# Optimization experiments

Measured on AMD Instinct MI355X. Metric: run time of the kernel, lower is better.

The kernel has to match this reference:

```python
import jax, jax.numpy as jnp
import numpy as np

EPS = 1e-5
NEG_INF = -9e15  # matches torch's -9000000000000000.0 mask fill


def layer_norm(x, g, b):
    mu = jnp.mean(x, axis=-1, keepdims=True)
    var = jnp.mean((x - mu) ** 2, axis=-1, keepdims=True)
    return (x - mu) / jnp.sqrt(var + EPS) * g + b


def setup_inputs() -> dict:
    key = jax.random.key(0)
    n, C, Cout, K = 8192, 128, 128, 2
    ks = jax.random.split(key, 5)
    x = jax.random.normal(ks[0], (n, C), dtype=jnp.float32)
    adj = jax.random.randint(ks[1], (n, n), 0, 2).astype(jnp.float32)  # 0/1 adjacency
    s = 1.0 / np.sqrt(C)
    # W0[i]: applied as h = x @ W0[i]  (== torch Linear(C,C,bias=False))
    W0 = jax.random.uniform(ks[2], (K, C, C), dtype=jnp.float32, minval=-s, maxval=s)
    W1 = jax.random.uniform(ks[3], (K, C, Cout), dtype=jnp.float32, minval=-s, maxval=s)
    sa = 1.0 / np.sqrt(2 * C)
    a = jax.random.uniform(ks[4], (K, 2 * C), dtype=jnp.float32, minval=-sa, maxval=sa)
    ln1_g = jnp.ones((C,), jnp.float32); ln1_b = jnp.zeros((C,), jnp.float32)
    ln2_g = jnp.ones((C,), jnp.float32); ln2_b = jnp.zeros((C,), jnp.float32)
    return {"x": x, "adj": adj, "W0": W0, "W1": W1, "a": a,
            "ln1_g": ln1_g, "ln1_b": ln1_b, "ln2_g": ln2_g, "ln2_b": ln2_b}


def reference(x, adj, W0, W1, a, ln1_g, ln1_b, ln2_g, ln2_b):
    n, C = x.shape
    K = W0.shape[0]
    Cout = W1.shape[-1]
    # adj + eye (repeated) only feeds `> 0`; equivalent fixed mask:
    mask = (adj > 0) | jnp.eye(n, dtype=bool)
    x_norm = layer_norm(x, ln1_g, ln1_b)
    h_next = jnp.zeros((n, Cout), dtype=x.dtype)
    atten_agg = jnp.zeros((n, n), dtype=x.dtype)
    for i in range(K):
        h = x_norm @ W0[i]                                   # (n, C)
        a_l, a_r = a[i, :C], a[i, C:]
        # h_cross[i,j] = [h[i], h[j]]; linear decomposes exactly:
        e = jax.nn.leaky_relu(h @ a_l[:, None] + (h @ a_r)[None, :])  # (n, n)
        e = jnp.where(mask, e, NEG_INF)
        atten = jax.nn.softmax(e, axis=1)                    # row-stochastic
        attn_h = atten @ h                                   # (n, C)
        attn_h = attn_h + x                                  # residual=True
        attn_h = layer_norm(attn_h, ln2_g, ln2_b)
        h_next = h_next + jax.nn.elu(attn_h @ W1[i]) / K
        atten_agg = atten_agg + atten / K
    return h_next, atten_agg
```

## Files before the change

kernel.cpp:

```cpp
#include <hip/hip_runtime.h>
#include <stdint.h>

#define N 8192
#define C 128

typedef float f32x4 __attribute__((ext_vector_type(4)));
typedef short bf16x8 __attribute__((ext_vector_type(8)));

__device__ __forceinline__ float wred(float v){
#pragma unroll
  for(int o=32;o;o>>=1) v += __shfl_xor(v,o);
  return v;
}
__device__ __forceinline__ unsigned short f2bf(float x){
  union{float f; unsigned u;} c; c.f = x;
  unsigned u = c.u;
  u += 0x7fffu + ((u>>16)&1u);
  return (unsigned short)(u>>16);
}
__device__ __forceinline__ float lrelu(float z){ return z>0.f ? z : 0.01f*z; }

__global__ void k_front(const float* __restrict__ x, const float* __restrict__ g1,
                        const float* __restrict__ b1, const float* __restrict__ W0,
                        const float* __restrict__ a, unsigned short* __restrict__ hB,
                        float* __restrict__ hl, float* __restrict__ hr){
  __shared__ __align__(16) float xn[32*132];
  __shared__ __align__(16) float ws[C*C];
  __shared__ __align__(16) float hs[32*C];
  int t = threadIdx.x, l = t & 63, w = t >> 6;
  int r0 = blockIdx.x*32;
#pragma unroll
  for(int p=0;p<8;p++){
    int row = p*4 + w;
    const float2 xv = *(const float2*)(x + (size_t)(r0+row)*C + l*2);
    float mu = wred(xv.x + xv.y) * (1.f/C);
    float dx = xv.x - mu, dy = xv.y - mu;
    float var = wred(dx*dx + dy*dy) * (1.f/C);
    float rs = rsqrtf(var + 1e-5f);
    const float2 gv = *(const float2*)(g1 + l*2);
    const float2 bv = *(const float2*)(b1 + l*2);
    xn[row*132 + l*2]     = dx*rs*gv.x + bv.x;
    xn[row*132 + l*2 + 1] = dy*rs*gv.y + bv.y;
  }
  int cq = t & 31, rq = t >> 5;
  for(int k=0;k<2;k++){
    __syncthreads();
    const float4* wsrc = (const float4*)(W0 + (size_t)k*C*C);
    float4* wdst = (float4*)ws;
#pragma unroll
    for(int r=0;r<16;r++) wdst[t + r*256] = wsrc[t + r*256];
    __syncthreads();
    float4 acc[4] = {};
    const float4* ws4 = (const float4*)ws;
#pragma unroll 4
    for(int kk=0; kk<C; ++kk){
      float4 wv = ws4[kk*32 + cq];
#pragma unroll
      for(int r=0;r<4;r++){
        float xv = xn[(rq*4+r)*132 + kk];
        acc[r].x += xv*wv.x; acc[r].y += xv*wv.y; acc[r].z += xv*wv.z; acc[r].w += xv*wv.w;
      }
    }
    const float4 al = *(const float4*)(a + k*2*C + cq*4);
    const float4 ar = *(const float4*)(a + k*2*C + C + cq*4);
#pragma unroll
    for(int r=0;r<4;r++){
      float sl = acc[r].x*al.x + acc[r].y*al.y + acc[r].z*al.z + acc[r].w*al.w;
      float sr = acc[r].x*ar.x + acc[r].y*ar.y + acc[r].z*ar.z + acc[r].w*ar.w;
#pragma unroll
      for(int o=16;o;o>>=1){ sl += __shfl_xor(sl,o); sr += __shfl_xor(sr,o); }
      if(cq==0){
        hl[k*N + r0 + rq*4 + r] = sl;
        hr[k*N + r0 + rq*4 + r] = sr;
      }
    }
#pragma unroll
    for(int r=0;r<4;r++) *(float4*)(hs + (rq*4+r)*C + cq*4) = acc[r];
    __syncthreads();
    unsigned short tv[16];
#pragma unroll
    for(int q=0;q<16;q++){
      int f = t*16 + q;
      int cb = f>>9, l2 = (f>>3)&63, tt = f&7;
      tv[q] = f2bf(hs[((l2>>4)*8 + tt)*C + cb*16 + (l2&15)]);
    }
    uint4* dst = (uint4*)(hB + (size_t)(k*256 + blockIdx.x)*4096 + t*16);
    dst[0] = *(uint4*)&tv[0];
    dst[1] = *(uint4*)&tv[8];
  }
}

__global__ void k_denom(const float* __restrict__ adj, const float* __restrict__ hl,
                        const float* __restrict__ hr, float* __restrict__ invd,
                        unsigned char* __restrict__ maskG){
  int t = threadIdx.x, l = t & 63, w = t >> 6;
  int i = blockIdx.x*8 + w;
  float hl0 = hl[i], hl1 = hl[N+i];
  const float4* arow = (const float4*)(adj + (size_t)i*N);
  float s0 = 0.f, s1 = 0.f;
  for(int it=0; it<16; ++it){
    int j0 = it*512 + l*8;
    float4 a0 = arow[j0/4], a1 = arow[j0/4 + 1];
    float4 h00 = *(const float4*)(hr + j0);
    float4 h01 = *(const float4*)(hr + j0 + 4);
    float4 h10 = *(const float4*)(hr + N + j0);
    float4 h11 = *(const float4*)(hr + N + j0 + 4);
    float av[8]  = {a0.x,a0.y,a0.z,a0.w, a1.x,a1.y,a1.z,a1.w};
    float h0v[8] = {h00.x,h00.y,h00.z,h00.w, h01.x,h01.y,h01.z,h01.w};
    float h1v[8] = {h10.x,h10.y,h10.z,h10.w, h11.x,h11.y,h11.z,h11.w};
    unsigned mb = 0;
#pragma unroll
    for(int tt=0; tt<8; ++tt){
      bool m = (av[tt] > 0.f) || (j0+tt == i);
      mb |= ((unsigned)m) << tt;
      float e0 = __expf(lrelu(hl0 + h0v[tt]));
      float e1 = __expf(lrelu(hl1 + h1v[tt]));
      s0 += m ? e0 : 0.f;
      s1 += m ? e1 : 0.f;
    }
    maskG[(size_t)i*1024 + it*64 + l] = (unsigned char)mb;
  }
  s0 = wred(s0); s1 = wred(s1);
  if(l==0){ invd[i] = 1.f/s0; invd[N+i] = 1.f/s1; }
}

__global__ __launch_bounds__(512, 4)
void k_main(const unsigned char* __restrict__ maskG, const float* __restrict__ hl,
            const float* __restrict__ hr, const float* __restrict__ invd,
            const unsigned short* __restrict__ hB,
            float* __restrict__ agg, float* __restrict__ pvp){
  __shared__ __align__(16) uint4 hBs[2][1024];
  __shared__ __align__(16) float hrs[2048];
  __shared__ __align__(16) unsigned char mlds[128*144];
  int t = threadIdx.x, l = t & 63, w = t >> 6;
  int r0 = blockIdx.x*128, ch = blockIdx.y;
  int g = l >> 4;
  int lr = w*16 + (l & 15);
  int i = r0 + lr;
  {
    int f0 = t*4, k0 = f0 >> 10, j0 = f0 & 1023;
    *(float4*)(hrs + f0) = *(const float4*)(hr + k0*N + ch*1024 + j0);
    const uint4* msrc = (const uint4*)(maskG + (size_t)(r0 + (t>>2))*1024 + ch*128 + (t&3)*32);
    uint4* mdst = (uint4*)(mlds + (t>>2)*144 + (t&3)*32);
    mdst[0] = msrc[0];
    mdst[1] = msrc[1];
  }
  float hl0 = hl[i], hl1 = hl[N+i];
  float id0 = invd[i], id1 = invd[N+i];
  float* grow = agg + (size_t)i*N;
  const uint4* hBu = (const uint4*)hB;
  f32x4 acc[2][8] = {};
  uint4 s0v, s1v;
  {
    size_t jn = (size_t)(ch*32)*512;
    s0v = hBu[jn + t];
    s1v = hBu[131072 + jn + t];
  }
  __syncthreads();
  int cur = 0;
  for(int js=0; js<32; ++js){
    int jblk = ch*32 + js;
    uint4* dstb = &hBs[cur][0];
    dstb[t      ] = s0v;
    dstb[t + 512] = s1v;
    if(js < 31){
      size_t jn = (size_t)(jblk+1)*512;
      s0v = hBu[jn + t];
      s1v = hBu[131072 + jn + t];
    }
    __syncthreads();
    int jb = jblk*32 + g*8;
    int jl = js*32 + g*8;
    float4 h00 = *(const float4*)(hrs + jl);
    float4 h01 = *(const float4*)(hrs + jl + 4);
    float4 h10 = *(const float4*)(hrs + 1024 + jl);
    float4 h11 = *(const float4*)(hrs + 1024 + jl + 4);
    unsigned mb = mlds[lr*144 + js*4 + g];
    float h0v[8] = {h00.x,h00.y,h00.z,h00.w, h01.x,h01.y,h01.z,h01.w};
    float h1v[8] = {h10.x,h10.y,h10.z,h10.w, h11.x,h11.y,h11.z,h11.w};
    float p0[8], p1[8];
#pragma unroll
    for(int tt=0; tt<8; ++tt){
      bool m = (mb >> tt) & 1;
      float e0 = __expf(lrelu(hl0 + h0v[tt]));
      float e1 = __expf(lrelu(hl1 + h1v[tt]));
      p0[tt] = m ? e0 : 0.f;
      p1[tt] = m ? e1 : 0.f;
    }
    float4 g0, g1;
    g0.x = (p0[0]*id0 + p1[0]*id1)*0.5f;
    g0.y = (p0[1]*id0 + p1[1]*id1)*0.5f;
    g0.z = (p0[2]*id0 + p1[2]*id1)*0.5f;
    g0.w = (p0[3]*id0 + p1[3]*id1)*0.5f;
    g1.x = (p0[4]*id0 + p1[4]*id1)*0.5f;
    g1.y = (p0[5]*id0 + p1[5]*id1)*0.5f;
    g1.z = (p0[6]*id0 + p1[6]*id1)*0.5f;
    g1.w = (p0[7]*id0 + p1[7]*id1)*0.5f;
    *(float4*)(grow + jb)     = g0;
    *(float4*)(grow + jb + 4) = g1;
    union { bf16x8 v; unsigned u[4]; } fu0, fu1;
#pragma unroll
    for(int q=0;q<4;q++){
      asm("v_cvt_pk_bf16_f32 %0, %1, %2" : "=v"(fu0.u[q]) : "v"(p0[2*q]), "v"(p0[2*q+1]));
      asm("v_cvt_pk_bf16_f32 %0, %1, %2" : "=v"(fu1.u[q]) : "v"(p1[2*q]), "v"(p1[2*q+1]));
    }
    const unsigned short* bptr = (const unsigned short*)&hBs[cur][0];
#pragma unroll
    for(int cb=0; cb<8; ++cb){
      bf16x8 b0 = *(const bf16x8*)(bptr + (cb*64 + l)*8);
      bf16x8 b1 = *(const bf16x8*)(bptr + 4096 + (cb*64 + l)*8);
      acc[0][cb] = __builtin_amdgcn_mfma_f32_16x16x32_bf16(fu0.v, b0, acc[0][cb], 0, 0, 0);
      acc[1][cb] = __builtin_amdgcn_mfma_f32_16x16x32_bf16(fu1.v, b1, acc[1][cb], 0, 0, 0);
    }
    __syncthreads();
    cur ^= 1;
  }
#pragma unroll
  for(int k=0;k<2;k++)
#pragma unroll
    for(int cb=0;cb<8;cb++)
#pragma unroll
      for(int r=0;r<4;r++){
        int ig = r0 + w*16 + ((l>>4)<<2) + r;
        int c = cb*16 + (l & 15);
        pvp[(size_t)((ch*2 + k)*N + ig)*C + c] = acc[k][cb][r];
      }
}

__global__ void k_reduce_ln(const float* __restrict__ pvp, const float* __restrict__ invd,
                            const float* __restrict__ x, const float* __restrict__ g2,
                            const float* __restrict__ b2, float* __restrict__ tmp){
  int l = threadIdx.x & 63, w = threadIdx.x >> 6;
  int wid = blockIdx.x*4 + w;
  int k = wid >> 13, i = wid & (N-1);
  float s0 = 0.f, s1 = 0.f;
#pragma unroll
  for(int ch=0; ch<8; ++ch){
    const float2 v = *(const float2*)(pvp + (size_t)((ch*2+k)*N + i)*C + l*2);
    s0 += v.x; s1 += v.y;
  }
  float idv = invd[k*N + i];
  const float2 xv = *(const float2*)(x + (size_t)i*C + l*2);
  float a0 = s0*idv + xv.x, a1 = s1*idv + xv.y;
  float mu = wred(a0 + a1) * (1.f/C);
  float d0 = a0 - mu, d1 = a1 - mu;
  float var = wred(d0*d0 + d1*d1) * (1.f/C);
  float rs = rsqrtf(var + 1e-5f);
  const float2 gv = *(const float2*)(g2 + l*2);
  const float2 bv = *(const float2*)(b2 + l*2);
  float2 o; o.x = d0*rs*gv.x + bv.x; o.y = d1*rs*gv.y + bv.y;
  *(float2*)(tmp + (size_t)k*N*C + (size_t)i*C + l*2) = o;
}

__global__ void k_out(const float* __restrict__ tmp, const float* __restrict__ W1,
                      float* __restrict__ out){
  __shared__ __align__(16) float ws[C*C];
  __shared__ __align__(16) float xs[32*132];
  int t = threadIdx.x, r0 = blockIdx.x*32;
  int cq = t & 31, rq = t >> 5;
  float oacc[4][4] = {};
  for(int k=0;k<2;k++){
    __syncthreads();
    const float4* wsrc = (const float4*)(W1 + (size_t)k*C*C);
    float4* wdst = (float4*)ws;
#pragma unroll
    for(int r=0;r<16;r++) wdst[t + r*256] = wsrc[t + r*256];
    const float4* xsrc = (const float4*)(tmp + (size_t)k*N*C + (size_t)r0*C);
#pragma unroll
    for(int r=0;r<4;r++){
      int f = t + r*256;
      int row = f >> 5, c4 = f & 31;
      *(float4*)(xs + row*132 + c4*4) = xsrc[f];
    }
    __syncthreads();
    float4 acc[4] = {};
    const float4* ws4 = (const float4*)ws;
#pragma unroll 4
    for(int kk=0; kk<C; ++kk){
      float4 wv = ws4[kk*32 + cq];
#pragma unroll
      for(int r=0;r<4;r++){
        float xv = xs[(rq*4+r)*132 + kk];
        acc[r].x += xv*wv.x; acc[r].y += xv*wv.y; acc[r].z += xv*wv.z; acc[r].w += xv*wv.w;
      }
    }
#pragma unroll
    for(int r=0;r<4;r++){
      float* ac = (float*)&acc[r];
#pragma unroll
      for(int cc=0;cc<4;cc++){
        float v = ac[cc];
        v = v > 0.f ? v : (__expf(v) - 1.f);
        oacc[r][cc] += 0.5f*v;
      }
    }
  }
#pragma unroll
  for(int r=0;r<4;r++){
    float4 o = make_float4(oacc[r][0], oacc[r][1], oacc[r][2], oacc[r][3]);
    *(float4*)(out + (size_t)(r0+rq*4+r)*C + cq*4) = o;
  }
}

extern "C" void kernel_launch(void* const* d_in, const int* in_sizes, int n_in,
                              void* d_out, int out_size, void* d_ws, size_t ws_size,
                              hipStream_t stream){
  const float* x   = (const float*)d_in[0];
  const float* adj = (const float*)d_in[1];
  const float* W0  = (const float*)d_in[2];
  const float* W1  = (const float*)d_in[3];
  const float* a   = (const float*)d_in[4];
  const float* g1  = (const float*)d_in[5];
  const float* b1  = (const float*)d_in[6];
  const float* g2  = (const float*)d_in[7];
  const float* b2  = (const float*)d_in[8];
  float* out = (float*)d_out;
  float* ws  = (float*)d_ws;

  unsigned short* hB = (unsigned short*)ws;
  float* hl   = ws + 1048576;
  float* hr   = ws + 1064960;
  float* invd = ws + 1081344;
  float* tmp  = ws + 1097728;
  float* pvp  = ws + 3194880;
  unsigned char* maskG = (unsigned char*)(ws + 19972096);
  float* agg  = out + (size_t)N*C;

  k_front    <<<N/32, 256, 0, stream>>>(x, g1, b1, W0, a, hB, hl, hr);
  k_denom    <<<N/8, 512, 0, stream>>>(adj, hl, hr, invd, maskG);
  k_main     <<<dim3(64, 8), 512, 0, stream>>>(maskG, hl, hr, invd, hB, agg, pvp);
  k_reduce_ln<<<(2*N)/4, 256, 0, stream>>>(pvp, invd, x, g2, b2, tmp);
  k_out      <<<N/32, 256, 0, stream>>>(tmp, W1, out);
}
```

Baseline: 270.0 us.

## Halve column split in attention kernel and restructure hB double-buffer pipeline

```diff
diff --git a/kernel.cpp b/kernel.cpp
--- a/kernel.cpp
+++ b/kernel.cpp
@@ -130,52 +130,44 @@
             const unsigned short* __restrict__ hB,
             float* __restrict__ agg, float* __restrict__ pvp){
   __shared__ __align__(16) uint4 hBs[2][1024];
-  __shared__ __align__(16) float hrs[2048];
-  __shared__ __align__(16) unsigned char mlds[128*144];
+  __shared__ __align__(16) float hrs[4096];
   int t = threadIdx.x, l = t & 63, w = t >> 6;
   int r0 = blockIdx.x*128, ch = blockIdx.y;
   int g = l >> 4;
   int lr = w*16 + (l & 15);
   int i = r0 + lr;
   {
-    int f0 = t*4, k0 = f0 >> 10, j0 = f0 & 1023;
-    *(float4*)(hrs + f0) = *(const float4*)(hr + k0*N + ch*1024 + j0);
-    const uint4* msrc = (const uint4*)(maskG + (size_t)(r0 + (t>>2))*1024 + ch*128 + (t&3)*32);
-    uint4* mdst = (uint4*)(mlds + (t>>2)*144 + (t&3)*32);
-    mdst[0] = msrc[0];
-    mdst[1] = msrc[1];
+    int f0 = t*8, k0 = f0 >> 11, j0 = f0 & 2047;
+    *(float4*)(hrs + f0)     = *(const float4*)(hr + k0*N + ch*2048 + j0);
+    *(float4*)(hrs + f0 + 4) = *(const float4*)(hr + k0*N + ch*2048 + j0 + 4);
   }
   float hl0 = hl[i], hl1 = hl[N+i];
   float id0 = invd[i], id1 = invd[N+i];
-  float* grow = agg + (size_t)i*N;
+  float* grow = agg + (size_t)i*N + ch*2048;
+  const unsigned char* mrow = maskG + (size_t)i*1024 + ch*256;
   const uint4* hBu = (const uint4*)hB;
   f32x4 acc[2][8] = {};
-  uint4 s0v, s1v;
   {
-    size_t jn = (size_t)(ch*32)*512;
-    s0v = hBu[jn + t];
-    s1v = hBu[131072 + jn + t];
-  }
+    size_t jn = (size_t)(ch*64)*512;
+    hBs[0][t]       = hBu[jn + t];
+    hBs[0][t + 512] = hBu[131072 + jn + t];
+  }
+  uint4 rB0, rB1;
+  {
+    size_t jn = (size_t)(ch*64 + 1)*512;
+    rB0 = hBu[jn + t];
+    rB1 = hBu[131072 + jn + t];
+  }
+  unsigned mb  = mrow[g];
+  unsigned mbn = mrow[4 + g];
   __syncthreads();
-  int cur = 0;
-  for(int js=0; js<32; ++js){
-    int jblk = ch*32 + js;
-    uint4* dstb = &hBs[cur][0];
-    dstb[t      ] = s0v;
-    dstb[t + 512] = s1v;
-    if(js < 31){
-      size_t jn = (size_t)(jblk+1)*512;
-      s0v = hBu[jn + t];
-      s1v = hBu[131072 + jn + t];
-    }
-    __syncthreads();
-    int jb = jblk*32 + g*8;
+  for(int js=0; js<64; ++js){
+    int cur = js & 1;
     int jl = js*32 + g*8;
     float4 h00 = *(const float4*)(hrs + jl);
     float4 h01 = *(const float4*)(hrs + jl + 4);
-    float4 h10 = *(const float4*)(hrs + 1024 + jl);
-    float4 h11 = *(const float4*)(hrs + 1024 + jl + 4);
-    unsigned mb = mlds[lr*144 + js*4 + g];
+    float4 h10 = *(const float4*)(hrs + 2048 + jl);
+    float4 h11 = *(const float4*)(hrs + 2048 + jl + 4);
     float h0v[8] = {h00.x,h00.y,h00.z,h00.w, h01.x,h01.y,h01.z,h01.w};
     float h1v[8] = {h10.x,h10.y,h10.z,h10.w, h11.x,h11.y,h11.z,h11.w};
     float p0[8], p1[8];
@@ -196,8 +188,8 @@
     g1.y = (p0[5]*id0 + p1[5]*id1)*0.5f;
     g1.z = (p0[6]*id0 + p1[6]*id1)*0.5f;
     g1.w = (p0[7]*id0 + p1[7]*id1)*0.5f;
-    *(float4*)(grow + jb)     = g0;
-    *(float4*)(grow + jb + 4) = g1;
+    *(float4*)(grow + jl)     = g0;
+    *(float4*)(grow + jl + 4) = g1;
     union { bf16x8 v; unsigned u[4]; } fu0, fu1;
 #pragma unroll
     for(int q=0;q<4;q++){
@@ -212,8 +204,20 @@
       acc[0][cb] = __builtin_amdgcn_mfma_f32_16x16x32_bf16(fu0.v, b0, acc[0][cb], 0, 0, 0);
       acc[1][cb] = __builtin_amdgcn_mfma_f32_16x16x32_bf16(fu1.v, b1, acc[1][cb], 0, 0, 0);
     }
-    __syncthreads();
-    cur ^= 1;
+    if(js < 63){
+      uint4* dstb = &hBs[cur ^ 1][0];
+      dstb[t]       = rB0;
+      dstb[t + 512] = rB1;
+    }
+    unsigned mbn2 = 0;
+    if(js < 62){
+      size_t jn = (size_t)(ch*64 + js + 2)*512;
+      rB0 = hBu[jn + t];
+      rB1 = hBu[131072 + jn + t];
+      mbn2 = mrow[(js+2)*4 + g];
+    }
+    mb = mbn; mbn = mbn2;
+    __syncthreads();
   }
 #pragma unroll
   for(int k=0;k<2;k++)
@@ -235,7 +239,7 @@
   int k = wid >> 13, i = wid & (N-1);
   float s0 = 0.f, s1 = 0.f;
 #pragma unroll
-  for(int ch=0; ch<8; ++ch){
+  for(int ch=0; ch<4; ++ch){
     const float2 v = *(const float2*)(pvp + (size_t)((ch*2+k)*N + i)*C + l*2);
     s0 += v.x; s1 += v.y;
   }
@@ -328,7 +332,7 @@
 
   k_front    <<<N/32, 256, 0, stream>>>(x, g1, b1, W0, a, hB, hl, hr);
   k_denom    <<<N/8, 512, 0, stream>>>(adj, hl, hr, invd, maskG);
-  k_main     <<<dim3(64, 8), 512, 0, stream>>>(maskG, hl, hr, invd, hB, agg, pvp);
+  k_main     <<<dim3(64, 4), 512, 0, stream>>>(maskG, hl, hr, invd, hB, agg, pvp);
   k_reduce_ln<<<(2*N)/4, 256, 0, stream>>>(pvp, invd, x, g2, b2, tmp);
   k_out      <<<N/32, 256, 0, stream>>>(tmp, W1, out);
 }
```

Measured after the change: 274.3 us. About the same (+1.6%).

## Deepen hB prefetch pipeline, single barrier per step, widen denom loop

Applied to the files above, without the earlier changes.

```diff
diff --git a/kernel.cpp b/kernel.cpp
--- a/kernel.cpp
+++ b/kernel.cpp
@@ -98,27 +98,30 @@
   float hl0 = hl[i], hl1 = hl[N+i];
   const float4* arow = (const float4*)(adj + (size_t)i*N);
   float s0 = 0.f, s1 = 0.f;
-  for(int it=0; it<16; ++it){
-    int j0 = it*512 + l*8;
-    float4 a0 = arow[j0/4], a1 = arow[j0/4 + 1];
-    float4 h00 = *(const float4*)(hr + j0);
-    float4 h01 = *(const float4*)(hr + j0 + 4);
-    float4 h10 = *(const float4*)(hr + N + j0);
-    float4 h11 = *(const float4*)(hr + N + j0 + 4);
-    float av[8]  = {a0.x,a0.y,a0.z,a0.w, a1.x,a1.y,a1.z,a1.w};
-    float h0v[8] = {h00.x,h00.y,h00.z,h00.w, h01.x,h01.y,h01.z,h01.w};
-    float h1v[8] = {h10.x,h10.y,h10.z,h10.w, h11.x,h11.y,h11.z,h11.w};
+  for(int it=0; it<8; ++it){
+    int j0 = it*1024 + l*16;
+    float4 a0 = arow[j0/4], a1 = arow[j0/4+1], a2 = arow[j0/4+2], a3 = arow[j0/4+3];
+    float4 p0 = *(const float4*)(hr + j0),     p1 = *(const float4*)(hr + j0 + 4);
+    float4 p2 = *(const float4*)(hr + j0 + 8), p3 = *(const float4*)(hr + j0 + 12);
+    float4 q0 = *(const float4*)(hr + N + j0),     q1 = *(const float4*)(hr + N + j0 + 4);
+    float4 q2 = *(const float4*)(hr + N + j0 + 8), q3 = *(const float4*)(hr + N + j0 + 12);
+    float avf[16] = {a0.x,a0.y,a0.z,a0.w, a1.x,a1.y,a1.z,a1.w,
+                     a2.x,a2.y,a2.z,a2.w, a3.x,a3.y,a3.z,a3.w};
+    float h0f[16] = {p0.x,p0.y,p0.z,p0.w, p1.x,p1.y,p1.z,p1.w,
+                     p2.x,p2.y,p2.z,p2.w, p3.x,p3.y,p3.z,p3.w};
+    float h1f[16] = {q0.x,q0.y,q0.z,q0.w, q1.x,q1.y,q1.z,q1.w,
+                     q2.x,q2.y,q2.z,q2.w, q3.x,q3.y,q3.z,q3.w};
     unsigned mb = 0;
 #pragma unroll
-    for(int tt=0; tt<8; ++tt){
-      bool m = (av[tt] > 0.f) || (j0+tt == i);
+    for(int tt=0; tt<16; ++tt){
+      bool m = (avf[tt] > 0.f) || (j0+tt == i);
       mb |= ((unsigned)m) << tt;
-      float e0 = __expf(lrelu(hl0 + h0v[tt]));
-      float e1 = __expf(lrelu(hl1 + h1v[tt]));
+      float e0 = __expf(lrelu(hl0 + h0f[tt]));
+      float e1 = __expf(lrelu(hl1 + h1f[tt]));
       s0 += m ? e0 : 0.f;
       s1 += m ? e1 : 0.f;
     }
-    maskG[(size_t)i*1024 + it*64 + l] = (unsigned char)mb;
+    *(unsigned short*)(maskG + (size_t)i*1024 + it*128 + l*2) = (unsigned short)mb;
   }
   s0 = wred(s0); s1 = wred(s1);
   if(l==0){ invd[i] = 1.f/s0; invd[N+i] = 1.f/s1; }
@@ -147,29 +150,33 @@
   }
   float hl0 = hl[i], hl1 = hl[N+i];
   float id0 = invd[i], id1 = invd[N+i];
-  float* grow = agg + (size_t)i*N;
+  float* grow = agg + (size_t)i*N + ch*1024;
   const uint4* hBu = (const uint4*)hB;
   f32x4 acc[2][8] = {};
-  uint4 s0v, s1v;
   {
     size_t jn = (size_t)(ch*32)*512;
-    s0v = hBu[jn + t];
-    s1v = hBu[131072 + jn + t];
+    hBs[0][t]       = hBu[jn + t];
+    hBs[0][t + 512] = hBu[131072 + jn + t];
+  }
+  uint4 rA0, rA1, rB0, rB1;
+  {
+    size_t jn = (size_t)(ch*32 + 1)*512;
+    rA0 = hBu[jn + t];
+    rA1 = hBu[131072 + jn + t];
   }
   __syncthreads();
   int cur = 0;
-  for(int js=0; js<32; ++js){
-    int jblk = ch*32 + js;
-    uint4* dstb = &hBs[cur][0];
-    dstb[t      ] = s0v;
-    dstb[t + 512] = s1v;
+  auto iter = [&](int js, uint4& c0, uint4& c1, uint4& n0, uint4& n1){
+    if(js < 30){
+      size_t jn = (size_t)(ch*32 + js + 2)*512;
+      n0 = hBu[jn + t];
+      n1 = hBu[131072 + jn + t];
+    }
     if(js < 31){
-      size_t jn = (size_t)(jblk+1)*512;
-      s0v = hBu[jn + t];
-      s1v = hBu[131072 + jn + t];
-    }
-    __syncthreads();
-    int jb = jblk*32 + g*8;
+      uint4* dstb = &hBs[cur ^ 1][0];
+      dstb[t]       = c0;
+      dstb[t + 512] = c1;
+    }
     int jl = js*32 + g*8;
     float4 h00 = *(const float4*)(hrs + jl);
     float4 h01 = *(const float4*)(hrs + jl + 4);
@@ -187,6 +194,20 @@
       p0[tt] = m ? e0 : 0.f;
       p1[tt] = m ? e1 : 0.f;
     }
+    union { bf16x8 v; unsigned u[4]; } fu0, fu1;
+#pragma unroll
+    for(int q=0;q<4;q++){
+      asm("v_cvt_pk_bf16_f32 %0, %1, %2" : "=v"(fu0.u[q]) : "v"(p0[2*q]), "v"(p0[2*q+1]));
+      asm("v_cvt_pk_bf16_f32 %0, %1, %2" : "=v"(fu1.u[q]) : "v"(p1[2*q]), "v"(p1[2*q+1]));
+    }
+    const unsigned short* bptr = (const unsigned short*)&hBs[cur][0];
+#pragma unroll
+    for(int cb=0; cb<8; ++cb){
+      bf16x8 b0 = *(const bf16x8*)(bptr + (cb*64 + l)*8);
+      bf16x8 b1 = *(const bf16x8*)(bptr + 4096 + (cb*64 + l)*8);
+      acc[0][cb] = __builtin_amdgcn_mfma_f32_16x16x32_bf16(fu0.v, b0, acc[0][cb], 0, 0, 0);
+      acc[1][cb] = __builtin_amdgcn_mfma_f32_16x16x32_bf16(fu1.v, b1, acc[1][cb], 0, 0, 0);
+    }
     float4 g0, g1;
     g0.x = (p0[0]*id0 + p1[0]*id1)*0.5f;
     g0.y = (p0[1]*id0 + p1[1]*id1)*0.5f;
@@ -196,24 +217,17 @@
     g1.y = (p0[5]*id0 + p1[5]*id1)*0.5f;
     g1.z = (p0[6]*id0 + p1[6]*id1)*0.5f;
     g1.w = (p0[7]*id0 + p1[7]*id1)*0.5f;
-    *(float4*)(grow + jb)     = g0;
-    *(float4*)(grow + jb + 4) = g1;
-    union { bf16x8 v; unsigned u[4]; } fu0, fu1;
-#pragma unroll
-    for(int q=0;q<4;q++){
-      asm("v_cvt_pk_bf16_f32 %0, %1, %2" : "=v"(fu0.u[q]) : "v"(p0[2*q]), "v"(p0[2*q+1]));
-      asm("v_cvt_pk_bf16_f32 %0, %1, %2" : "=v"(fu1.u[q]) : "v"(p1[2*q]), "v"(p1[2*q+1]));
-    }
-    const unsigned short* bptr = (const unsigned short*)&hBs[cur][0];
-#pragma unroll
-    for(int cb=0; cb<8; ++cb){
-      bf16x8 b0 = *(const bf16x8*)(bptr + (cb*64 + l)*8);
-      bf16x8 b1 = *(const bf16x8*)(bptr + 4096 + (cb*64 + l)*8);
-      acc[0][cb] = __builtin_amdgcn_mfma_f32_16x16x32_bf16(fu0.v, b0, acc[0][cb], 0, 0, 0);
-      acc[1][cb] = __builtin_amdgcn_mfma_f32_16x16x32_bf16(fu1.v, b1, acc[1][cb], 0, 0, 0);
-    }
-    __syncthreads();
+    *(float4*)(grow + jl)     = g0;
+    *(float4*)(grow + jl + 4) = g1;
+    asm volatile("s_waitcnt lgkmcnt(0)" ::: "memory");
+    __builtin_amdgcn_sched_barrier(0);
+    __builtin_amdgcn_s_barrier();
+    __builtin_amdgcn_sched_barrier(0);
     cur ^= 1;
+  };
+  for(int js=0; js<32; js+=2){
+    iter(js,   rA0, rA1, rB0, rB1);
+    iter(js+1, rB0, rB1, rA0, rA1);
   }
 #pragma unroll
   for(int k=0;k<2;k++)
```

After: 283.6 us. +5.0%, slower.

## Fuse reduce+LayerNorm into output GEMM, widen denom loads, remap main grid

Applied to the files above, without the earlier changes.

```diff
diff --git a/kernel.cpp b/kernel.cpp
--- a/kernel.cpp
+++ b/kernel.cpp
@@ -98,27 +98,30 @@
   float hl0 = hl[i], hl1 = hl[N+i];
   const float4* arow = (const float4*)(adj + (size_t)i*N);
   float s0 = 0.f, s1 = 0.f;
-  for(int it=0; it<16; ++it){
-    int j0 = it*512 + l*8;
-    float4 a0 = arow[j0/4], a1 = arow[j0/4 + 1];
-    float4 h00 = *(const float4*)(hr + j0);
-    float4 h01 = *(const float4*)(hr + j0 + 4);
-    float4 h10 = *(const float4*)(hr + N + j0);
-    float4 h11 = *(const float4*)(hr + N + j0 + 4);
-    float av[8]  = {a0.x,a0.y,a0.z,a0.w, a1.x,a1.y,a1.z,a1.w};
-    float h0v[8] = {h00.x,h00.y,h00.z,h00.w, h01.x,h01.y,h01.z,h01.w};
-    float h1v[8] = {h10.x,h10.y,h10.z,h10.w, h11.x,h11.y,h11.z,h11.w};
+  for(int it=0; it<8; ++it){
+    int j0 = it*1024 + l*16;
+    float4 a0 = arow[j0/4], a1 = arow[j0/4+1], a2 = arow[j0/4+2], a3 = arow[j0/4+3];
+    float4 p0 = *(const float4*)(hr + j0),     p1 = *(const float4*)(hr + j0 + 4);
+    float4 p2 = *(const float4*)(hr + j0 + 8), p3 = *(const float4*)(hr + j0 + 12);
+    float4 q0 = *(const float4*)(hr + N + j0),     q1 = *(const float4*)(hr + N + j0 + 4);
+    float4 q2 = *(const float4*)(hr + N + j0 + 8), q3 = *(const float4*)(hr + N + j0 + 12);
+    float avf[16] = {a0.x,a0.y,a0.z,a0.w, a1.x,a1.y,a1.z,a1.w,
+                     a2.x,a2.y,a2.z,a2.w, a3.x,a3.y,a3.z,a3.w};
+    float h0f[16] = {p0.x,p0.y,p0.z,p0.w, p1.x,p1.y,p1.z,p1.w,
+                     p2.x,p2.y,p2.z,p2.w, p3.x,p3.y,p3.z,p3.w};
+    float h1f[16] = {q0.x,q0.y,q0.z,q0.w, q1.x,q1.y,q1.z,q1.w,
+                     q2.x,q2.y,q2.z,q2.w, q3.x,q3.y,q3.z,q3.w};
     unsigned mb = 0;
 #pragma unroll
-    for(int tt=0; tt<8; ++tt){
-      bool m = (av[tt] > 0.f) || (j0+tt == i);
+    for(int tt=0; tt<16; ++tt){
+      bool m = (avf[tt] > 0.f) || (j0+tt == i);
       mb |= ((unsigned)m) << tt;
-      float e0 = __expf(lrelu(hl0 + h0v[tt]));
-      float e1 = __expf(lrelu(hl1 + h1v[tt]));
+      float e0 = __expf(lrelu(hl0 + h0f[tt]));
+      float e1 = __expf(lrelu(hl1 + h1f[tt]));
       s0 += m ? e0 : 0.f;
       s1 += m ? e1 : 0.f;
     }
-    maskG[(size_t)i*1024 + it*64 + l] = (unsigned char)mb;
+    *(unsigned short*)(maskG + (size_t)i*1024 + it*128 + l*2) = (unsigned short)mb;
   }
   s0 = wred(s0); s1 = wred(s1);
   if(l==0){ invd[i] = 1.f/s0; invd[N+i] = 1.f/s1; }
@@ -133,7 +136,9 @@
   __shared__ __align__(16) float hrs[2048];
   __shared__ __align__(16) unsigned char mlds[128*144];
   int t = threadIdx.x, l = t & 63, w = t >> 6;
-  int r0 = blockIdx.x*128, ch = blockIdx.y;
+  int bid = blockIdx.x;
+  int ch = bid & 7, rtile = bid >> 3;
+  int r0 = rtile*128;
   int g = l >> 4;
   int lr = w*16 + (l & 15);
   int i = r0 + lr;
@@ -227,36 +232,14 @@
       }
 }
 
-__global__ void k_reduce_ln(const float* __restrict__ pvp, const float* __restrict__ invd,
-                            const float* __restrict__ x, const float* __restrict__ g2,
-                            const float* __restrict__ b2, float* __restrict__ tmp){
-  int l = threadIdx.x & 63, w = threadIdx.x >> 6;
-  int wid = blockIdx.x*4 + w;
-  int k = wid >> 13, i = wid & (N-1);
-  float s0 = 0.f, s1 = 0.f;
-#pragma unroll
-  for(int ch=0; ch<8; ++ch){
-    const float2 v = *(const float2*)(pvp + (size_t)((ch*2+k)*N + i)*C + l*2);
-    s0 += v.x; s1 += v.y;
-  }
-  float idv = invd[k*N + i];
-  const float2 xv = *(const float2*)(x + (size_t)i*C + l*2);
-  float a0 = s0*idv + xv.x, a1 = s1*idv + xv.y;
-  float mu = wred(a0 + a1) * (1.f/C);
-  float d0 = a0 - mu, d1 = a1 - mu;
-  float var = wred(d0*d0 + d1*d1) * (1.f/C);
-  float rs = rsqrtf(var + 1e-5f);
-  const float2 gv = *(const float2*)(g2 + l*2);
-  const float2 bv = *(const float2*)(b2 + l*2);
-  float2 o; o.x = d0*rs*gv.x + bv.x; o.y = d1*rs*gv.y + bv.y;
-  *(float2*)(tmp + (size_t)k*N*C + (size_t)i*C + l*2) = o;
-}
-
-__global__ void k_out(const float* __restrict__ tmp, const float* __restrict__ W1,
-                      float* __restrict__ out){
+__global__ void k_tail(const float* __restrict__ pvp, const float* __restrict__ invd,
+                       const float* __restrict__ x, const float* __restrict__ g2,
+                       const float* __restrict__ b2, const float* __restrict__ W1,
+                       float* __restrict__ out){
   __shared__ __align__(16) float ws[C*C];
   __shared__ __align__(16) float xs[32*132];
-  int t = threadIdx.x, r0 = blockIdx.x*32;
+  int t = threadIdx.x, l = t & 63, w = t >> 6;
+  int r0 = blockIdx.x*32;
   int cq = t & 31, rq = t >> 5;
   float oacc[4][4] = {};
   for(int k=0;k<2;k++){
@@ -265,12 +248,27 @@
     float4* wdst = (float4*)ws;
 #pragma unroll
     for(int r=0;r<16;r++) wdst[t + r*256] = wsrc[t + r*256];
-    const float4* xsrc = (const float4*)(tmp + (size_t)k*N*C + (size_t)r0*C);
-#pragma unroll
-    for(int r=0;r<4;r++){
-      int f = t + r*256;
-      int row = f >> 5, c4 = f & 31;
-      *(float4*)(xs + row*132 + c4*4) = xsrc[f];
+#pragma unroll
+    for(int p=0;p<8;p++){
+      int row = p*4 + w;
+      int i = r0 + row;
+      float s0 = 0.f, s1 = 0.f;
+#pragma unroll
+      for(int ch=0; ch<8; ++ch){
+        const float2 v = *(const float2*)(pvp + (size_t)((ch*2+k)*N + i)*C + l*2);
+        s0 += v.x; s1 += v.y;
+      }
+      float idv = invd[k*N + i];
+      const float2 xv = *(const float2*)(x + (size_t)i*C + l*2);
+      float a0 = s0*idv + xv.x, a1 = s1*idv + xv.y;
+      float mu = wred(a0 + a1) * (1.f/C);
+      float d0 = a0 - mu, d1 = a1 - mu;
+      float var = wred(d0*d0 + d1*d1) * (1.f/C);
+      float rs = rsqrtf(var + 1e-5f);
+      const float2 gv = *(const float2*)(g2 + l*2);
+      const float2 bv = *(const float2*)(b2 + l*2);
+      xs[row*132 + l*2]     = d0*rs*gv.x + bv.x;
+      xs[row*132 + l*2 + 1] = d1*rs*gv.y + bv.y;
     }
     __syncthreads();
     float4 acc[4] = {};
@@ -321,14 +319,12 @@
   float* hl   = ws + 1048576;
   float* hr   = ws + 1064960;
   float* invd = ws + 1081344;
-  float* tmp  = ws + 1097728;
   float* pvp  = ws + 3194880;
   unsigned char* maskG = (unsigned char*)(ws + 19972096);
   float* agg  = out + (size_t)N*C;
 
-  k_front    <<<N/32, 256, 0, stream>>>(x, g1, b1, W0, a, hB, hl, hr);
-  k_denom    <<<N/8, 512, 0, stream>>>(adj, hl, hr, invd, maskG);
-  k_main     <<<dim3(64, 8), 512, 0, stream>>>(maskG, hl, hr, invd, hB, agg, pvp);
-  k_reduce_ln<<<(2*N)/4, 256, 0, stream>>>(pvp, invd, x, g2, b2, tmp);
-  k_out      <<<N/32, 256, 0, stream>>>(tmp, W1, out);
-}
+  k_front <<<N/32, 256, 0, stream>>>(x, g1, b1, W0, a, hB, hl, hr);
+  k_denom <<<N/8, 512, 0, stream>>>(adj, hl, hr, invd, maskG);
+  k_main  <<<512, 512, 0, stream>>>(maskG, hl, hr, invd, hB, agg, pvp);
+  k_tail  <<<N/32, 256, 0, stream>>>(pvp, invd, x, g2, b2, W1, out);
+}
```

Result: slower. 354.9 us (+31.5%).
